# Optimization experiments

Hardware: AMD Instinct MI355X
Metric: run time of the kernel (lower is better)

Reference implementation:

```python
import jax, jax.numpy as jnp
import numpy as np

B, T, H = 8, 2048, 2048
N = 100000
PROJ = 512
TOP_K = 10
LN_EPS = 1e-5


def setup_inputs() -> dict:
    key = jax.random.key(0)
    ks = jax.random.split(key, 16)
    s = 0.02
    return {
        "x": jax.random.normal(ks[0], (B, T, H), jnp.float32),
        "keys": jax.random.normal(ks[1], (N, H), jnp.float32),
        "confidences": jax.random.uniform(ks[2], (N,), jnp.float32),
        "Wq": jax.random.normal(ks[3], (PROJ, H), jnp.float32) * s,
        "bq": jnp.zeros((PROJ,), jnp.float32),
        "Wk": jax.random.normal(ks[4], (PROJ, H), jnp.float32) * s,
        "bk": jnp.zeros((PROJ,), jnp.float32),
        "Wg": jax.random.normal(ks[5], (H, 2 * H), jnp.float32) * s,
        "bg": jnp.zeros((H,), jnp.float32),
        "Wm1": jax.random.normal(ks[6], (H, 2 * H), jnp.float32) * s,
        "bm1": jnp.zeros((H,), jnp.float32),
        "Wm2": jax.random.normal(ks[7], (H, H), jnp.float32) * s,
        "bm2": jnp.zeros((H,), jnp.float32),
        "gamma": jnp.ones((H,), jnp.float32),
        "beta": jnp.zeros((H,), jnp.float32),
    }


def reference(x, keys, confidences, Wq, bq, Wk, bk, Wg, bg, Wm1, bm1, Wm2, bm2, gamma, beta):
    # query = mean over time: (B, H)
    query = x.mean(axis=1)
    # projections
    q = query @ Wq.T + bq                  # (B, 512)
    k_proj = keys @ Wk.T + bk              # (N, 512)
    # confidence-scaled scores and top-k retrieval
    scores = (q @ k_proj.T) * confidences[None, :]   # (B, N)
    _, top_idx = jax.lax.top_k(scores, TOP_K)        # (B, k)
    retrieved = keys[top_idx]                        # (B, k, H) gather
    mem_summary = retrieved.mean(axis=1)             # (B, H)
    gate_input = jnp.concatenate([query, mem_summary], axis=-1)  # (B, 2H)
    gate = jax.nn.sigmoid(gate_input @ Wg.T + bg)[:, None, :]    # (B, 1, H)
    h = jax.nn.gelu(gate_input @ Wm1.T + bm1, approximate=False)
    mem_integrated = (h @ Wm2.T + bm2)[:, None, :]               # (B, 1, H)
    y = x + gate * mem_integrated
    # LayerNorm over last dim
    mu = y.mean(axis=-1, keepdims=True)
    var = jnp.mean(jnp.square(y - mu), axis=-1, keepdims=True)
    return (y - mu) * jax.lax.rsqrt(var + LN_EPS) * gamma + beta
```

## Files before the change

kernel.cpp:

```cpp
#include <hip/hip_runtime.h>
#include <math.h>

constexpr int B    = 8;
constexpr int T    = 2048;
constexpr int H    = 2048;
constexpr int NK   = 100000;
constexpr int PROJ = 512;
constexpr int TOPK = 10;
constexpr int TCHUNK = 64;
constexpr int TSUB   = T / TCHUNK;
constexpr int NCHUNK = 64;
constexpr int CS     = 1600;

#define NEG_INF -3.4e38f

typedef float vfloat4 __attribute__((ext_vector_type(4)));
typedef float vfloat2 __attribute__((ext_vector_type(2)));

__global__ void __launch_bounds__(256) k_partial_sum(const float* __restrict__ x,
                                                     float* __restrict__ partial) {
    int hblk = blockIdx.x & 1;
    int tc   = (blockIdx.x >> 1) & 63;
    int b    = blockIdx.x >> 7;
    int h    = hblk * 1024 + threadIdx.x * 4;
    const float* xp = x + ((size_t)b * T + (size_t)tc * TSUB) * H + h;
    vfloat4 acc = {0.f, 0.f, 0.f, 0.f};
#pragma unroll 4
    for (int t = 0; t < TSUB; ++t) {
        vfloat4 v = *(const vfloat4*)(xp + (size_t)t * H);
        acc += v;
    }
    *(vfloat4*)(partial + ((size_t)(b * TCHUNK + tc)) * H + h) = acc;
}

__global__ void __launch_bounds__(256) k_finish_mean(const float* __restrict__ partial,
                                                     float* __restrict__ query,
                                                     float* __restrict__ gi) {
    int idx = blockIdx.x * 256 + threadIdx.x;
    int b = idx >> 11, h = idx & 2047;
    float s = 0.f;
#pragma unroll 8
    for (int tc = 0; tc < TCHUNK; ++tc)
        s += partial[((size_t)(b * TCHUNK + tc)) * H + h];
    float m = s * (1.0f / T);
    query[idx] = m;
    gi[(size_t)b * 2 * H + h] = m;
}

__global__ void __launch_bounds__(256) k_q(const float* __restrict__ query,
                                           const float* __restrict__ Wq,
                                           const float* __restrict__ bq,
                                           float* __restrict__ qv) {
    int wave = threadIdx.x >> 6, lane = threadIdx.x & 63;
    int gidx = blockIdx.x * 4 + wave;
    int b = gidx >> 9, p = gidx & 511;
    const float* qr = query + (size_t)b * H;
    const float* wr = Wq + (size_t)p * H;
    float acc = 0.f;
#pragma unroll 2
    for (int j = lane * 4; j < H; j += 256) {
        float4 a = *(const float4*)(qr + j);
        float4 w = *(const float4*)(wr + j);
        acc += a.x * w.x + a.y * w.y + a.z * w.z + a.w * w.w;
    }
    for (int o = 32; o > 0; o >>= 1) acc += __shfl_down(acc, o, 64);
    if (lane == 0) qv[gidx] = acc + bq[p];
}

__global__ void __launch_bounds__(256) k_qk_partial(const float* __restrict__ qv,
                                                    const float* __restrict__ Wk,
                                                    const float* __restrict__ bk,
                                                    float* __restrict__ pqk,
                                                    float* __restrict__ qb) {
    if (blockIdx.x == 128) {
        int lane = threadIdx.x & 63;
        if (threadIdx.x < 64) {
            for (int b = 0; b < B; ++b) {
                float acc = 0.f;
                for (int j = lane; j < PROJ; j += 64) acc += qv[b * PROJ + j] * bk[j];
                for (int o = 32; o > 0; o >>= 1) acc += __shfl_down(acc, o, 64);
                if (lane == 0) qb[b] = acc;
            }
        }
        return;
    }
    int hblk = blockIdx.x & 7, pc = blockIdx.x >> 3;
    int h = hblk * 256 + threadIdx.x;
    float acc[B];
#pragma unroll
    for (int b = 0; b < B; ++b) acc[b] = 0.f;
#pragma unroll 4
    for (int p = pc * 32; p < pc * 32 + 32; ++p) {
        float w = Wk[(size_t)p * H + h];
#pragma unroll
        for (int b = 0; b < B; ++b) acc[b] += qv[b * PROJ + p] * w;
    }
#pragma unroll
    for (int b = 0; b < B; ++b)
        pqk[((size_t)(pc * B + b)) * H + h] = acc[b];
}

__global__ void __launch_bounds__(256) k_qk_finish(const float* __restrict__ pqk,
                                                   float* __restrict__ qk) {
    int idx = blockIdx.x * 256 + threadIdx.x;
    int b = idx >> 11, h = idx & 2047;
    float s = 0.f;
#pragma unroll 8
    for (int pc = 0; pc < 16; ++pc) s += pqk[((size_t)(pc * B + b)) * H + h];
    qk[idx] = s;
}

__global__ void __launch_bounds__(512) k_scores(const float* __restrict__ keys,
                                                const float* __restrict__ conf,
                                                const float* __restrict__ qk,
                                                const float* __restrict__ qb,
                                                float* __restrict__ scores) {
    __shared__ float sqk[B * H];
    for (int i = threadIdx.x * 4; i < B * H; i += 2048)
        *(vfloat4*)(sqk + i) = *(const vfloat4*)(qk + i);
    __syncthreads();

    const int wave = threadIdx.x >> 6, lane = threadIdx.x & 63;
    const long r0 = (long)blockIdx.x * 32 + wave * 4;

    vfloat2 acc[4][B];
#pragma unroll
    for (int r = 0; r < 4; ++r)
#pragma unroll
        for (int b = 0; b < B; ++b) acc[r][b] = (vfloat2){0.f, 0.f};

#pragma unroll 2
    for (int it = 0; it < 8; ++it) {
        int j = it * 256 + lane * 4;
        vfloat4 kv[4];
#pragma unroll
        for (int r = 0; r < 4; ++r)
            kv[r] = *(const vfloat4*)(keys + (size_t)(r0 + r) * H + j);
#pragma unroll
        for (int b = 0; b < B; ++b) {
            vfloat4 w = *(const vfloat4*)(sqk + b * H + j);
            vfloat2 wlo = w.xy, whi = w.zw;
#pragma unroll
            for (int r = 0; r < 4; ++r) {
                acc[r][b] += kv[r].xy * wlo;
                acc[r][b] += kv[r].zw * whi;
            }
        }
    }

#pragma unroll
    for (int r = 0; r < 4; ++r) {
        long n = r0 + r;
#pragma unroll
        for (int b = 0; b < B; ++b) {
            float v = acc[r][b].x + acc[r][b].y;
            for (int o = 32; o > 0; o >>= 1) v += __shfl_down(v, o, 64);
            if (lane == 0)
                scores[(size_t)b * NK + n] = conf[n] * (v + qb[b]);
        }
    }
}

__global__ void __launch_bounds__(256) k_topk1(const float* __restrict__ scores,
                                               float* __restrict__ candv,
                                               int* __restrict__ candi) {
    const int c = blockIdx.x & (NCHUNK - 1), b = blockIdx.x >> 6;
    const int tid = threadIdx.x, lane = tid & 63, wave = tid >> 6;
    __shared__ float wv[4 * TOPK];
    __shared__ int   wi[4 * TOPK];

    float lv[TOPK];
    int   li[TOPK];
#pragma unroll
    for (int i = 0; i < TOPK; ++i) { lv[i] = NEG_INF; li[i] = 0; }

    const int start = c * CS;
    const int end = (start + CS < NK) ? start + CS : NK;
    for (int n = start + tid; n < end; n += 256) {
        float v = scores[(size_t)b * NK + n];
        if (v > lv[TOPK - 1]) {
            bool m[TOPK];
#pragma unroll
            for (int i = 0; i < TOPK; ++i) m[i] = (lv[i] < v);
#pragma unroll
            for (int i = TOPK - 1; i > 0; --i)
                if (m[i - 1]) { lv[i] = lv[i - 1]; li[i] = li[i - 1]; }
#pragma unroll
            for (int i = 0; i < TOPK; ++i)
                if (m[i] && (i == 0 || !m[i - 1])) { lv[i] = v; li[i] = n; }
        }
    }

    for (int round = 0; round < TOPK; ++round) {
        float bv = lv[0]; int bi = li[0]; int bl = lane;
        for (int o = 32; o > 0; o >>= 1) {
            float ov = __shfl_down(bv, o, 64);
            int   oi = __shfl_down(bi, o, 64);
            int   ol = __shfl_down(bl, o, 64);
            if (ov > bv) { bv = ov; bi = oi; bl = ol; }
        }
        if (lane == 0) { wv[wave * TOPK + round] = bv; wi[wave * TOPK + round] = bi; }
        bl = __shfl(bl, 0, 64);
        if (lane == bl) {
#pragma unroll
            for (int i = 0; i < TOPK - 1; ++i) { lv[i] = lv[i + 1]; li[i] = li[i + 1]; }
            lv[TOPK - 1] = NEG_INF;
        }
    }
    __syncthreads();

    if (wave == 0) {
        float v = (lane < 4 * TOPK) ? wv[lane] : NEG_INF;
        int  id = (lane < 4 * TOPK) ? wi[lane] : 0;
        for (int round = 0; round < TOPK; ++round) {
            float bv = v; int bi = id; int bl = lane;
            for (int o = 32; o > 0; o >>= 1) {
                float ov = __shfl_down(bv, o, 64);
                int   oi = __shfl_down(bi, o, 64);
                int   ol = __shfl_down(bl, o, 64);
                if (ov > bv) { bv = ov; bi = oi; bl = ol; }
            }
            if (lane == 0) {
                candv[(size_t)(b * NCHUNK + c) * TOPK + round] = bv;
                candi[(size_t)(b * NCHUNK + c) * TOPK + round] = bi;
            }
            bl = __shfl(bl, 0, 64);
            if (lane == bl) v = NEG_INF;
        }
    }
}

__global__ void __launch_bounds__(256) k_memsum(const float* __restrict__ keys,
                                                const float* __restrict__ candv,
                                                const int* __restrict__ candi,
                                                float* __restrict__ gi) {
    const int blk = blockIdx.x;
    const int b = (blk * 256) >> 11;
    const int tid = threadIdx.x, lane = tid & 63, wave = tid >> 6;
    __shared__ int stop[TOPK];

    if (wave == 0) {
        float lv[TOPK];
        int   li[TOPK];
#pragma unroll
        for (int r = 0; r < TOPK; ++r) {
            lv[r] = candv[(size_t)(b * NCHUNK + lane) * TOPK + r];
            li[r] = candi[(size_t)(b * NCHUNK + lane) * TOPK + r];
        }
        for (int round = 0; round < TOPK; ++round) {
            float bv = lv[0]; int bi = li[0]; int bl = lane;
            for (int o = 32; o > 0; o >>= 1) {
                float ov = __shfl_down(bv, o, 64);
                int   oi = __shfl_down(bi, o, 64);
                int   ol = __shfl_down(bl, o, 64);
                if (ov > bv) { bv = ov; bi = oi; bl = ol; }
            }
            if (lane == 0) stop[round] = bi;
            bl = __shfl(bl, 0, 64);
            if (lane == bl) {
#pragma unroll
                for (int i = 0; i < TOPK - 1; ++i) { lv[i] = lv[i + 1]; li[i] = li[i + 1]; }
                lv[TOPK - 1] = NEG_INF;
            }
        }
    }
    __syncthreads();

    int h = (blk * 256 + tid) & 2047;
    float s = 0.f;
#pragma unroll
    for (int i = 0; i < TOPK; ++i) {
        int n = stop[i];
        s += keys[(size_t)n * H + h];
    }
    gi[(size_t)b * 2 * H + H + h] = s * (1.0f / TOPK);
}

__global__ void __launch_bounds__(256) k_mlp1(const float* __restrict__ gi,
                                              const float* __restrict__ Wg,
                                              const float* __restrict__ bg,
                                              const float* __restrict__ Wm1,
                                              const float* __restrict__ bm1,
                                              float* __restrict__ gate,
                                              float* __restrict__ h1) {
    int wave = threadIdx.x >> 6, lane = threadIdx.x & 63;
    int row = blockIdx.x * 4 + wave;
    bool isGate = row < H;
    int i = isGate ? row : row - H;
    const float* W = (isGate ? Wg : Wm1) + (size_t)i * 2 * H;

    float acc[B];
#pragma unroll
    for (int b = 0; b < B; ++b) acc[b] = 0.f;

#pragma unroll 2
    for (int j = lane * 4; j < 2 * H; j += 256) {
        float4 w = *(const float4*)(W + j);
#pragma unroll
        for (int b = 0; b < B; ++b) {
            float4 g = *(const float4*)(gi + (size_t)b * 2 * H + j);
            acc[b] += w.x * g.x + w.y * g.y + w.z * g.z + w.w * g.w;
        }
    }
#pragma unroll
    for (int b = 0; b < B; ++b) {
        float v = acc[b];
        for (int o = 32; o > 0; o >>= 1) v += __shfl_down(v, o, 64);
        if (lane == 0) {
            if (isGate) {
                v += bg[i];
                gate[b * H + i] = 1.0f / (1.0f + expf(-v));
            } else {
                v += bm1[i];
                h1[b * H + i] = 0.5f * v * (1.0f + erff(v * 0.70710678118654752f));
            }
        }
    }
}

__global__ void __launch_bounds__(256) k_mlp2(const float* __restrict__ h1,
                                              const float* __restrict__ Wm2,
                                              const float* __restrict__ bm2,
                                              const float* __restrict__ gate,
                                              float* __restrict__ gm) {
    int wave = threadIdx.x >> 6, lane = threadIdx.x & 63;
    int o = blockIdx.x * 4 + wave;
    const float* W = Wm2 + (size_t)o * H;
    float acc[B];
#pragma unroll
    for (int b = 0; b < B; ++b) acc[b] = 0.f;
#pragma unroll 2
    for (int j = lane * 4; j < H; j += 256) {
        float4 w = *(const float4*)(W + j);
#pragma unroll
        for (int b = 0; b < B; ++b) {
            float4 hh = *(const float4*)(h1 + (size_t)b * H + j);
            acc[b] += w.x * hh.x + w.y * hh.y + w.z * hh.z + w.w * hh.w;
        }
    }
#pragma unroll
    for (int b = 0; b < B; ++b) {
        float v = acc[b];
        for (int oo = 32; oo > 0; oo >>= 1) v += __shfl_down(v, oo, 64);
        if (lane == 0) gm[b * H + o] = gate[b * H + o] * (v + bm2[o]);
    }
}

__global__ void __launch_bounds__(256) k_final(const float* __restrict__ x,
                                               const float* __restrict__ gm,
                                               const float* __restrict__ gamma,
                                               const float* __restrict__ beta,
                                               float* __restrict__ out) {
    const int lane = threadIdx.x & 63, wave = threadIdx.x >> 6;
    const size_t row = (size_t)blockIdx.x * 4 + wave;
    const int b = (int)(row >> 11);
    const float* xr  = x + row * H;
    const float* gmr = gm + (size_t)b * H;

    vfloat4 y[8];
    float s = 0.f;
#pragma unroll
    for (int it = 0; it < 8; ++it) {
        int j = it * 256 + lane * 4;
        vfloat4 xv = *(const vfloat4*)(xr + j);
        vfloat4 gv = *(const vfloat4*)(gmr + j);
        y[it] = xv + gv;
        s += y[it].x + y[it].y + y[it].z + y[it].w;
    }
#pragma unroll
    for (int o = 32; o > 0; o >>= 1) s += __shfl_xor(s, o, 64);
    const float mu = s * (1.0f / H);

    float s2 = 0.f;
#pragma unroll
    for (int it = 0; it < 8; ++it) {
        vfloat4 d = y[it] - mu;
        y[it] = d;
        s2 += d.x * d.x + d.y * d.y + d.z * d.z + d.w * d.w;
    }
#pragma unroll
    for (int o = 32; o > 0; o >>= 1) s2 += __shfl_xor(s2, o, 64);
    const float inv = rsqrtf(s2 * (1.0f / H) + 1e-5f);

#pragma unroll
    for (int it = 0; it < 8; ++it) {
        int j = it * 256 + lane * 4;
        vfloat4 g = *(const vfloat4*)(gamma + j);
        vfloat4 bb = *(const vfloat4*)(beta + j);
        vfloat4 o_ = y[it] * inv * g + bb;
        __builtin_nontemporal_store(o_, (vfloat4*)(out + row * H + j));
    }
}

extern "C" void kernel_launch(void* const* d_in, const int* in_sizes, int n_in,
                              void* d_out, int out_size, void* d_ws, size_t ws_size,
                              hipStream_t stream) {
    const float* x     = (const float*)d_in[0];
    const float* keys  = (const float*)d_in[1];
    const float* conf  = (const float*)d_in[2];
    const float* Wq    = (const float*)d_in[3];
    const float* bq    = (const float*)d_in[4];
    const float* Wk    = (const float*)d_in[5];
    const float* bk    = (const float*)d_in[6];
    const float* Wg    = (const float*)d_in[7];
    const float* bg    = (const float*)d_in[8];
    const float* Wm1   = (const float*)d_in[9];
    const float* bm1   = (const float*)d_in[10];
    const float* Wm2   = (const float*)d_in[11];
    const float* bm2   = (const float*)d_in[12];
    const float* gamma = (const float*)d_in[13];
    const float* beta  = (const float*)d_in[14];
    float* out = (float*)d_out;

    float* ws = (float*)d_ws;
    float* partial = ws;        ws += (size_t)B * TCHUNK * H;
    float* query   = ws;        ws += B * H;
    float* gi      = ws;        ws += B * 2 * H;
    float* qv      = ws;        ws += B * PROJ;
    float* qb      = ws;        ws += 64;
    float* pqk     = ws;        ws += 16 * B * H;
    float* qk      = ws;        ws += B * H;
    float* scores  = ws;        ws += (size_t)B * NK;
    float* candv   = ws;        ws += B * NCHUNK * TOPK;
    int*   candi   = (int*)ws;  ws += B * NCHUNK * TOPK;
    float* gate    = ws;        ws += B * H;
    float* h1      = ws;        ws += B * H;
    float* gm      = ws;        ws += B * H;

    k_partial_sum<<<B * TCHUNK * 2, 256, 0, stream>>>(x, partial);
    k_finish_mean<<<B * H / 256, 256, 0, stream>>>(partial, query, gi);
    k_q<<<B * PROJ / 4, 256, 0, stream>>>(query, Wq, bq, qv);
    k_qk_partial<<<129, 256, 0, stream>>>(qv, Wk, bk, pqk, qb);
    k_qk_finish<<<B * H / 256, 256, 0, stream>>>(pqk, qk);
    k_scores<<<NK / 32, 512, 0, stream>>>(keys, conf, qk, qb, scores);
    k_topk1<<<B * NCHUNK, 256, 0, stream>>>(scores, candv, candi);
    k_memsum<<<B * H / 256, 256, 0, stream>>>(keys, candv, candi, gi);
    k_mlp1<<<2 * H / 4, 256, 0, stream>>>(gi, Wg, bg, Wm1, bm1, gate, h1);
    k_mlp2<<<H / 4, 256, 0, stream>>>(h1, Wm2, bm2, gate, gm);
    k_final<<<B * T / 4, 256, 0, stream>>>(x, gm, gamma, beta, out);
}
```

Baseline: 374.3 us.

## Fuse qk reduction and top-k merge/memsum via last-block atomic counter

Replaces the two-kernel split-P qk computation with a single kernel that loops over all 512 projection rows per output, removing the partial buffer and one launch. The final top-k merge and key gather-mean are folded into k_topk1, where the last block per batch (detected by an atomic counter reset in k_qk) does the merge. Key loads in k_scores become nontemporal. This trades two launches and an intermediate buffer for less parallelism in the qk kernel (65 blocks, serial 512-long loops) and a serialized tail in the last topk block.

After: 370.1 us. No clear change (-1.1%).

```diff
diff --git a/kernel.cpp b/kernel.cpp
--- a/kernel.cpp
+++ b/kernel.cpp
@@ -67,12 +67,13 @@
     if (lane == 0) qv[gidx] = acc + bq[p];
 }
 
-__global__ void __launch_bounds__(256) k_qk_partial(const float* __restrict__ qv,
-                                                    const float* __restrict__ Wk,
-                                                    const float* __restrict__ bk,
-                                                    float* __restrict__ pqk,
-                                                    float* __restrict__ qb) {
-    if (blockIdx.x == 128) {
+__global__ void __launch_bounds__(256) k_qk(const float* __restrict__ qv,
+                                            const float* __restrict__ Wk,
+                                            const float* __restrict__ bk,
+                                            float* __restrict__ qk,
+                                            float* __restrict__ qb,
+                                            int* __restrict__ cnt) {
+    if (blockIdx.x == 64) {
         int lane = threadIdx.x & 63;
         if (threadIdx.x < 64) {
             for (int b = 0; b < B; ++b) {
@@ -82,32 +83,17 @@
                 if (lane == 0) qb[b] = acc;
             }
         }
+        if (threadIdx.x < B) cnt[threadIdx.x] = 0;
         return;
     }
-    int hblk = blockIdx.x & 7, pc = blockIdx.x >> 3;
-    int h = hblk * 256 + threadIdx.x;
-    float acc[B];
-#pragma unroll
-    for (int b = 0; b < B; ++b) acc[b] = 0.f;
-#pragma unroll 4
-    for (int p = pc * 32; p < pc * 32 + 32; ++p) {
-        float w = Wk[(size_t)p * H + h];
-#pragma unroll
-        for (int b = 0; b < B; ++b) acc[b] += qv[b * PROJ + p] * w;
-    }
-#pragma unroll
-    for (int b = 0; b < B; ++b)
-        pqk[((size_t)(pc * B + b)) * H + h] = acc[b];
-}
-
-__global__ void __launch_bounds__(256) k_qk_finish(const float* __restrict__ pqk,
-                                                   float* __restrict__ qk) {
-    int idx = blockIdx.x * 256 + threadIdx.x;
-    int b = idx >> 11, h = idx & 2047;
-    float s = 0.f;
-#pragma unroll 8
-    for (int pc = 0; pc < 16; ++pc) s += pqk[((size_t)(pc * B + b)) * H + h];
-    qk[idx] = s;
+    int b = threadIdx.x >> 5;
+    int h = blockIdx.x * 32 + (threadIdx.x & 31);
+    const float* qrow = qv + b * PROJ;
+    float acc = 0.f;
+#pragma unroll 16
+    for (int p = 0; p < PROJ; ++p)
+        acc += qrow[p] * Wk[(size_t)p * H + h];
+    qk[b * H + h] = acc;
 }
 
 __global__ void __launch_bounds__(512) k_scores(const float* __restrict__ keys,
@@ -135,7 +121,8 @@
         vfloat4 kv[4];
 #pragma unroll
         for (int r = 0; r < 4; ++r)
-            kv[r] = *(const vfloat4*)(keys + (size_t)(r0 + r) * H + j);
+            kv[r] = __builtin_nontemporal_load(
+                (const vfloat4*)(keys + (size_t)(r0 + r) * H + j));
 #pragma unroll
         for (int b = 0; b < B; ++b) {
             vfloat4 w = *(const vfloat4*)(sqk + b * H + j);
@@ -162,12 +149,17 @@
 }
 
 __global__ void __launch_bounds__(256) k_topk1(const float* __restrict__ scores,
+                                               const float* __restrict__ keys,
                                                float* __restrict__ candv,
-                                               int* __restrict__ candi) {
+                                               int* __restrict__ candi,
+                                               int* __restrict__ cnt,
+                                               float* __restrict__ gi) {
     const int c = blockIdx.x & (NCHUNK - 1), b = blockIdx.x >> 6;
     const int tid = threadIdx.x, lane = tid & 63, wave = tid >> 6;
     __shared__ float wv[4 * TOPK];
     __shared__ int   wi[4 * TOPK];
+    __shared__ int   stop[TOPK];
+    __shared__ int   amLast;
 
     float lv[TOPK];
     int   li[TOPK];
@@ -228,27 +220,25 @@
             if (lane == bl) v = NEG_INF;
         }
     }
-}
-
-__global__ void __launch_bounds__(256) k_memsum(const float* __restrict__ keys,
-                                                const float* __restrict__ candv,
-                                                const int* __restrict__ candi,
-                                                float* __restrict__ gi) {
-    const int blk = blockIdx.x;
-    const int b = (blk * 256) >> 11;
-    const int tid = threadIdx.x, lane = tid & 63, wave = tid >> 6;
-    __shared__ int stop[TOPK];
+    __syncthreads();
+
+    if (tid == 0) {
+        __threadfence();
+        amLast = (atomicAdd(&cnt[b], 1) == NCHUNK - 1);
+    }
+    __syncthreads();
+    if (!amLast) return;
 
     if (wave == 0) {
-        float lv[TOPK];
-        int   li[TOPK];
+        float fv[TOPK];
+        int   fi[TOPK];
 #pragma unroll
         for (int r = 0; r < TOPK; ++r) {
-            lv[r] = candv[(size_t)(b * NCHUNK + lane) * TOPK + r];
-            li[r] = candi[(size_t)(b * NCHUNK + lane) * TOPK + r];
+            fv[r] = candv[(size_t)(b * NCHUNK + lane) * TOPK + r];
+            fi[r] = candi[(size_t)(b * NCHUNK + lane) * TOPK + r];
         }
         for (int round = 0; round < TOPK; ++round) {
-            float bv = lv[0]; int bi = li[0]; int bl = lane;
+            float bv = fv[0]; int bi = fi[0]; int bl = lane;
             for (int o = 32; o > 0; o >>= 1) {
                 float ov = __shfl_down(bv, o, 64);
                 int   oi = __shfl_down(bi, o, 64);
@@ -259,21 +249,22 @@
             bl = __shfl(bl, 0, 64);
             if (lane == bl) {
 #pragma unroll
-                for (int i = 0; i < TOPK - 1; ++i) { lv[i] = lv[i + 1]; li[i] = li[i + 1]; }
-                lv[TOPK - 1] = NEG_INF;
+                for (int i = 0; i < TOPK - 1; ++i) { fv[i] = fv[i + 1]; fi[i] = fi[i + 1]; }
+                fv[TOPK - 1] = NEG_INF;
             }
         }
     }
     __syncthreads();
 
-    int h = (blk * 256 + tid) & 2047;
-    float s = 0.f;
-#pragma unroll
-    for (int i = 0; i < TOPK; ++i) {
-        int n = stop[i];
-        s += keys[(size_t)n * H + h];
-    }
-    gi[(size_t)b * 2 * H + H + h] = s * (1.0f / TOPK);
+    for (int h = tid; h < H; h += 256) {
+        float s = 0.f;
+#pragma unroll
+        for (int i = 0; i < TOPK; ++i) {
+            int n = stop[i];
+            s += keys[(size_t)n * H + h];
+        }
+        gi[(size_t)b * 2 * H + H + h] = s * (1.0f / TOPK);
+    }
 }
 
 __global__ void __launch_bounds__(256) k_mlp1(const float* __restrict__ gi,
@@ -418,11 +409,11 @@
     float* gi      = ws;        ws += B * 2 * H;
     float* qv      = ws;        ws += B * PROJ;
     float* qb      = ws;        ws += 64;
-    float* pqk     = ws;        ws += 16 * B * H;
     float* qk      = ws;        ws += B * H;
     float* scores  = ws;        ws += (size_t)B * NK;
     float* candv   = ws;        ws += B * NCHUNK * TOPK;
     int*   candi   = (int*)ws;  ws += B * NCHUNK * TOPK;
+    int*   cnt     = (int*)ws;  ws += 64;
     float* gate    = ws;        ws += B * H;
     float* h1      = ws;        ws += B * H;
     float* gm      = ws;        ws += B * H;
@@ -430,11 +421,9 @@
     k_partial_sum<<<B * TCHUNK * 2, 256, 0, stream>>>(x, partial);
     k_finish_mean<<<B * H / 256, 256, 0, stream>>>(partial, query, gi);
     k_q<<<B * PROJ / 4, 256, 0, stream>>>(query, Wq, bq, qv);
-    k_qk_partial<<<129, 256, 0, stream>>>(qv, Wk, bk, pqk, qb);
-    k_qk_finish<<<B * H / 256, 256, 0, stream>>>(pqk, qk);
+    k_qk<<<65, 256, 0, stream>>>(qv, Wk, bk, qk, qb, cnt);
     k_scores<<<NK / 32, 512, 0, stream>>>(keys, conf, qk, qb, scores);
-    k_topk1<<<B * NCHUNK, 256, 0, stream>>>(scores, candv, candi);
-    k_memsum<<<B * H / 256, 256, 0, stream>>>(keys, candv, candi, gi);
+    k_topk1<<<B * NCHUNK, 256, 0, stream>>>(scores, keys, candv, candi, cnt, gi);
     k_mlp1<<<2 * H / 4, 256, 0, stream>>>(gi, Wg, bg, Wm1, bm1, gate, h1);
     k_mlp2<<<H / 4, 256, 0, stream>>>(h1, Wm2, bm2, gate, gm);
     k_final<<<B * T / 4, 256, 0, stream>>>(x, gm, gamma, beta, out);
```

## Restructure score kernel with double-buffered LDS key staging and register-resident queries

Applied to the files above, without the earlier changes.

Rewrites the key-score kernel so each wave keeps two batch query vectors in registers and reads key rows from a double-buffered LDS tile. The tile is filled with direct global-to-LDS async loads. This removes the 64KB shared query copy and overlaps key loading with compute. The cost is a block-wide barrier per chunk, LDS traffic for keys, and more shuffle reductions, since each wave now reduces 32 values.

Result: slower. 1.144 ms (+205.6%).

```diff
diff --git a/kernel.cpp b/kernel.cpp
--- a/kernel.cpp
+++ b/kernel.cpp
@@ -15,7 +15,12 @@
 #define NEG_INF -3.4e38f
 
 typedef float vfloat4 __attribute__((ext_vector_type(4)));
-typedef float vfloat2 __attribute__((ext_vector_type(2)));
+
+__device__ __forceinline__ void stage16(const float* gsrc, float* lds) {
+    __builtin_amdgcn_global_load_lds(
+        (const __attribute__((address_space(1))) void*)gsrc,
+        (__attribute__((address_space(3))) void*)lds, 16, 0, 0);
+}
 
 __global__ void __launch_bounds__(256) k_partial_sum(const float* __restrict__ x,
                                                      float* __restrict__ partial) {
@@ -115,48 +120,62 @@
                                                 const float* __restrict__ qk,
                                                 const float* __restrict__ qb,
                                                 float* __restrict__ scores) {
-    __shared__ float sqk[B * H];
-    for (int i = threadIdx.x * 4; i < B * H; i += 2048)
-        *(vfloat4*)(sqk + i) = *(const vfloat4*)(qk + i);
+    __shared__ float kbuf[2][32][256];
+    const int tid = threadIdx.x, wave = tid >> 6, lane = tid & 63;
+    const int bg = wave & 3, rh = wave >> 2;
+    const int b0 = 2 * bg, b1 = 2 * bg + 1;
+    const long r0 = (long)blockIdx.x * 32;
+
+    vfloat4 q0[8], q1[8];
+#pragma unroll
+    for (int c = 0; c < 8; ++c) {
+        q0[c] = *(const vfloat4*)(qk + (size_t)b0 * H + c * 256 + lane * 4);
+        q1[c] = *(const vfloat4*)(qk + (size_t)b1 * H + c * 256 + lane * 4);
+    }
+
+    float acc0[16], acc1[16];
+#pragma unroll
+    for (int r = 0; r < 16; ++r) { acc0[r] = 0.f; acc1[r] = 0.f; }
+
+#pragma unroll
+    for (int i = 0; i < 4; ++i) {
+        int row = 4 * wave + i;
+        stage16(keys + (size_t)(r0 + row) * H + lane * 4, &kbuf[0][row][0]);
+    }
     __syncthreads();
 
-    const int wave = threadIdx.x >> 6, lane = threadIdx.x & 63;
-    const long r0 = (long)blockIdx.x * 32 + wave * 4;
-
-    vfloat2 acc[4][B];
-#pragma unroll
-    for (int r = 0; r < 4; ++r)
-#pragma unroll
-        for (int b = 0; b < B; ++b) acc[r][b] = (vfloat2){0.f, 0.f};
-
-#pragma unroll 2
-    for (int it = 0; it < 8; ++it) {
-        int j = it * 256 + lane * 4;
-        vfloat4 kv[4];
-#pragma unroll
-        for (int r = 0; r < 4; ++r)
-            kv[r] = *(const vfloat4*)(keys + (size_t)(r0 + r) * H + j);
-#pragma unroll
-        for (int b = 0; b < B; ++b) {
-            vfloat4 w = *(const vfloat4*)(sqk + b * H + j);
-            vfloat2 wlo = w.xy, whi = w.zw;
-#pragma unroll
-            for (int r = 0; r < 4; ++r) {
-                acc[r][b] += kv[r].xy * wlo;
-                acc[r][b] += kv[r].zw * whi;
-            }
-        }
-    }
-
-#pragma unroll
-    for (int r = 0; r < 4; ++r) {
-        long n = r0 + r;
-#pragma unroll
-        for (int b = 0; b < B; ++b) {
-            float v = acc[r][b].x + acc[r][b].y;
-            for (int o = 32; o > 0; o >>= 1) v += __shfl_down(v, o, 64);
-            if (lane == 0)
-                scores[(size_t)b * NK + n] = conf[n] * (v + qb[b]);
+#pragma unroll
+    for (int c = 0; c < 8; ++c) {
+        if (c < 7) {
+#pragma unroll
+            for (int i = 0; i < 4; ++i) {
+                int row = 4 * wave + i;
+                stage16(keys + (size_t)(r0 + row) * H + (c + 1) * 256 + lane * 4,
+                        &kbuf[(c + 1) & 1][row][0]);
+            }
+        }
+#pragma unroll
+        for (int r = 0; r < 16; ++r) {
+            vfloat4 kv = *(const vfloat4*)(&kbuf[c & 1][rh * 16 + r][lane * 4]);
+            acc0[r] += kv.x * q0[c].x + kv.y * q0[c].y + kv.z * q0[c].z + kv.w * q0[c].w;
+            acc1[r] += kv.x * q1[c].x + kv.y * q1[c].y + kv.z * q1[c].z + kv.w * q1[c].w;
+        }
+        __syncthreads();
+    }
+
+    const float qb0 = qb[b0], qb1 = qb[b1];
+#pragma unroll
+    for (int r = 0; r < 16; ++r) {
+        long n = r0 + rh * 16 + r;
+        float v0 = acc0[r], v1 = acc1[r];
+        for (int o = 32; o > 0; o >>= 1) {
+            v0 += __shfl_down(v0, o, 64);
+            v1 += __shfl_down(v1, o, 64);
+        }
+        if (lane == 0) {
+            float cf = conf[n];
+            scores[(size_t)b0 * NK + n] = cf * (v0 + qb0);
+            scores[(size_t)b1 * NK + n] = cf * (v1 + qb1);
         }
     }
 }
```
